# Optimization experiments

Measured on AMD Instinct MI355X. Metric: run time of the kernel, lower is better.

## Reference

```python
import jax, jax.numpy as jnp
import numpy as np

Q, C, T, D_IN, D_H = 512, 512, 128, 512, 256


def setup_inputs() -> dict:
    key = jax.random.key(0)
    ks = jax.random.split(key, 8)
    s_in = 1.0 / np.sqrt(D_IN)
    s_h = 1.0 / np.sqrt(D_H)
    return {
        "audio": jax.random.normal(ks[0], (Q, T, D_IN), jnp.float32),
        "video": jax.random.normal(ks[1], (C, T, D_IN), jnp.float32),
        "a_w1": jax.random.normal(ks[2], (D_IN, D_H), jnp.float32) * s_in,
        "a_b1": jnp.zeros((D_H,), jnp.float32),
        "a_w2": jax.random.normal(ks[3], (D_H, D_H), jnp.float32) * s_h,
        "a_b2": jnp.zeros((D_H,), jnp.float32),
        "v_w1": jax.random.normal(ks[4], (D_IN, D_H), jnp.float32) * s_in,
        "v_b1": jnp.zeros((D_H,), jnp.float32),
        "v_w2": jax.random.normal(ks[5], (D_H, D_H), jnp.float32) * s_h,
        "v_b2": jnp.zeros((D_H,), jnp.float32),
        "W": jax.random.normal(ks[6], (D_H, D_H), jnp.float32) * s_h,
        "max_lag": 4,
    }


def _mlp(x, w1, b1, w2, b2):
    # Linear -> ReLU -> Linear
    h = jnp.maximum(x @ w1 + b1, 0.0)
    return h @ w2 + b2


def reference(audio, video, a_w1, a_b1, a_w2, a_b2,
              v_w1, v_b1, v_w2, v_b2, W, max_lag):
    a = _mlp(audio, a_w1, a_b1, a_w2, a_b2)   # [Q, T, D_H]
    v = _mlp(video, v_w1, v_b1, v_w2, v_b2)   # [C, T, D_H]
    # roll along time commutes with the per-frame linear map, so project once
    pv = jnp.einsum('ctd,df->ctf', v, W)      # [C, T, D_H]
    best = None
    for delta in range(-max_lag, max_lag + 1):
        shifted = jnp.roll(pv, delta, axis=1)
        score = jnp.einsum('qtd,ctd->qc', a, shifted)  # [Q, C]
        best = score if best is None else jnp.maximum(best, score)
    return best
```

## Files before the change

### kernel.cpp

```cpp
#include <hip/hip_runtime.h>
#include <cstdint>
#include <cstddef>

typedef __attribute__((ext_vector_type(8))) short frag8;
typedef __attribute__((ext_vector_type(4))) float f32x4;

static __device__ __forceinline__ unsigned short f2bf(float f) {
    unsigned int u = __float_as_uint(f);
    u += 0x7fffu + ((u >> 16) & 1u);
    return (unsigned short)(u >> 16);
}

static __device__ __forceinline__ void gll16(const void* g, void* l) {
    __builtin_amdgcn_global_load_lds(
        (const __attribute__((address_space(1))) unsigned int*)g,
        (__attribute__((address_space(3))) unsigned int*)l, 16, 0, 0);
}

#define CST 136

template<int AMODE, bool RELU>
__global__ __launch_bounds__(256, 2)
void gemm_mlp(const void* __restrict__ A0, const void* __restrict__ A1,
              const unsigned short* __restrict__ B0, const unsigned short* __restrict__ B1,
              const float* __restrict__ bias0, const float* __restrict__ bias1,
              unsigned short* __restrict__ C0, unsigned short* __restrict__ C1,
              int ldA, int kLen)
{
    __shared__ __align__(16) char smem[CST * 128 * 2];
    unsigned short* As = (unsigned short*)smem;
    unsigned short* Bs = (unsigned short*)(smem + (AMODE == 0 ? 10240 : 8192));
    unsigned short* Cst = (unsigned short*)smem;

    const void* Av = blockIdx.z ? A1 : A0;
    const unsigned short* Bt = blockIdx.z ? B1 : B0;
    const float* bias = blockIdx.z ? bias1 : bias0;
    unsigned short* Cv = blockIdx.z ? C1 : C0;

    const int t    = threadIdx.x;
    const int wave = t >> 6;
    const int lane = t & 63;
    const int quad = lane >> 4;
    const int l15  = lane & 15;
    const int wm   = (wave >> 1) * 64;
    const int wn   = (wave & 1) * 64;
    const int m0   = blockIdx.y * 128;
    const int n0   = blockIdx.x * 128;

    const int rowL = (wave << 5) + (lane >> 2);
    const int qL   = (lane & 3) ^ ((lane >> 3) & 3);
    const size_t offB0 = (size_t)(n0 + rowL) * kLen + qL * 8;
    const size_t offA0 = (size_t)(m0 + rowL) * ldA + qL * 8;
    const int swz = quad ^ ((l15 >> 1) & 3);

    f32x4 acc[4][4];
    #pragma unroll
    for (int i = 0; i < 4; ++i)
        #pragma unroll
        for (int j = 0; j < 4; ++j)
            acc[i][j] = (f32x4){0.f, 0.f, 0.f, 0.f};

    for (int k0 = 0; k0 < kLen; k0 += 32) {
        gll16(Bt + offB0 + k0, &Bs[wave * 1024]);
        gll16(Bt + offB0 + (size_t)16 * kLen + k0, &Bs[wave * 1024 + 512]);
        if (AMODE == 1) {
            const unsigned short* A = (const unsigned short*)Av;
            gll16(A + offA0 + k0, &As[wave * 1024]);
            gll16(A + offA0 + (size_t)16 * ldA + k0, &As[wave * 1024 + 512]);
        } else {
            const float* A = (const float*)Av;
            #pragma unroll
            for (int p = 0; p < 4; ++p) {
                int idx = p * 256 + t;
                int row = idx >> 3;
                int col = (idx & 7) * 4;
                const float4 v = *(const float4*)(A + (size_t)(m0 + row) * ldA + (k0 + col));
                unsigned int u0 = (unsigned int)f2bf(v.x) | ((unsigned int)f2bf(v.y) << 16);
                unsigned int u1 = (unsigned int)f2bf(v.z) | ((unsigned int)f2bf(v.w) << 16);
                uint2 pk; pk.x = u0; pk.y = u1;
                *(uint2*)&As[row * 40 + col] = pk;
            }
        }
        __syncthreads();

        frag8 af[4], bf[4];
        #pragma unroll
        for (int i = 0; i < 4; ++i) {
            const int row = wm + i * 16 + l15;
            if (AMODE == 0)
                af[i] = *(const frag8*)&As[row * 40 + quad * 8];
            else
                af[i] = *(const frag8*)&As[(row * 4 + swz) * 8];
        }
        #pragma unroll
        for (int j = 0; j < 4; ++j) {
            const int row = wn + j * 16 + l15;
            bf[j] = *(const frag8*)&Bs[(row * 4 + swz) * 8];
        }
        #pragma unroll
        for (int i = 0; i < 4; ++i)
            #pragma unroll
            for (int j = 0; j < 4; ++j)
                acc[i][j] = __builtin_amdgcn_mfma_f32_16x16x32_bf16(af[i], bf[j], acc[i][j], 0, 0, 0);
        __syncthreads();
    }

    #pragma unroll
    for (int i = 0; i < 4; ++i) {
        const int rl = wm + i * 16 + quad * 4;
        #pragma unroll
        for (int j = 0; j < 4; ++j) {
            const int cl = wn + j * 16 + l15;
            const float bv = bias[n0 + cl];
            #pragma unroll
            for (int r = 0; r < 4; ++r) {
                float val = acc[i][j][r] + bv;
                if (RELU) val = fmaxf(val, 0.0f);
                Cst[(rl + r) * CST + cl] = f2bf(val);
            }
        }
    }
    __syncthreads();
    #pragma unroll
    for (int u = 0; u < 8; ++u) {
        const int c   = u * 256 + t;
        const int row = c >> 4;
        const int c8  = (c & 15) * 8;
        uint4 v = *(const uint4*)&Cst[row * CST + c8];
        *(uint4*)&Cv[(size_t)(m0 + row) * 256 + n0 + c8] = v;
    }
}

__global__ __launch_bounds__(256, 2)
void gemm_corr(const unsigned short* __restrict__ A, const unsigned short* __restrict__ B,
               float* __restrict__ partial)
{
    __shared__ __align__(16) unsigned short As[128 * 64];
    __shared__ __align__(16) unsigned short Bs[128 * 64];

    const int t    = threadIdx.x;
    const int wave = t >> 6;
    const int lane = t & 63;
    const int quad = lane >> 4;
    const int l15  = lane & 15;
    const int wm   = (wave >> 1) * 64;
    const int wn   = (wave & 1) * 64;
    const int m0   = blockIdx.y * 128;
    const int n0   = blockIdx.x * 128;

    const int z      = blockIdx.z;
    const int kStart = (z & 3) * 8192;
    const int delta  = (z >> 2) - 4;
    const int koff   = (32768 - 256 * delta) & 32767;

    const int rowL = (wave << 5) + (lane >> 3);
    const int qL   = (lane & 7) ^ ((lane >> 3) & 7);
    const size_t aBase = (size_t)(m0 + rowL) * 32768 + qL * 8;
    const size_t bBase = (size_t)(n0 + rowL) * 32768 + qL * 8;
    unsigned short* AsW = As + wave * 2048;
    unsigned short* BsW = Bs + wave * 2048;
    const int swz = l15 & 7;

    f32x4 acc[4][4];
    #pragma unroll
    for (int i = 0; i < 4; ++i)
        #pragma unroll
        for (int j = 0; j < 4; ++j)
            acc[i][j] = (f32x4){0.f, 0.f, 0.f, 0.f};

    for (int k0 = 0; k0 < 8192; k0 += 64) {
        const int kA = kStart + k0;
        const int kB = (kA + koff) & 32767;
        #pragma unroll
        for (int p = 0; p < 4; ++p) {
            gll16(A + aBase + (size_t)(p * 8) * 32768 + kA, AsW + p * 512);
            gll16(B + bBase + (size_t)(p * 8) * 32768 + kB, BsW + p * 512);
        }
        __syncthreads();

        frag8 af[2][4], bf[2][4];
        #pragma unroll
        for (int i = 0; i < 4; ++i) {
            const int row = wm + i * 16 + l15;
            #pragma unroll
            for (int kh = 0; kh < 2; ++kh)
                af[kh][i] = *(const frag8*)&As[row * 64 + (((kh * 4 + quad) ^ swz) * 8)];
        }
        #pragma unroll
        for (int j = 0; j < 4; ++j) {
            const int row = wn + j * 16 + l15;
            #pragma unroll
            for (int kh = 0; kh < 2; ++kh)
                bf[kh][j] = *(const frag8*)&Bs[row * 64 + (((kh * 4 + quad) ^ swz) * 8)];
        }
        #pragma unroll
        for (int kh = 0; kh < 2; ++kh)
            #pragma unroll
            for (int i = 0; i < 4; ++i)
                #pragma unroll
                for (int j = 0; j < 4; ++j)
                    acc[i][j] = __builtin_amdgcn_mfma_f32_16x16x32_bf16(af[kh][i], bf[kh][j], acc[i][j], 0, 0, 0);
        __syncthreads();
    }

    float* C = partial + (size_t)z * 262144;
    #pragma unroll
    for (int i = 0; i < 4; ++i) {
        const int rg = m0 + wm + i * 16 + quad * 4;
        #pragma unroll
        for (int j = 0; j < 4; ++j) {
            const int cg = n0 + wn + j * 16 + l15;
            #pragma unroll
            for (int r = 0; r < 4; ++r)
                C[(size_t)(rg + r) * 512 + cg] = acc[i][j][r];
        }
    }
}

__global__ void prep(const float* __restrict__ a_w1, const float* __restrict__ v_w1,
                     const float* __restrict__ a_w2, const float* __restrict__ v_w2,
                     const float* __restrict__ W, const float* __restrict__ v_b2,
                     unsigned short* __restrict__ aw1T, unsigned short* __restrict__ vw1T,
                     unsigned short* __restrict__ aw2T,
                     unsigned short* __restrict__ WcT, float* __restrict__ bc)
{
    const int b = blockIdx.x;
    __shared__ float tl[32][33];
    __shared__ float wcol[256];
    if (b < 320) {
        const float* src; unsigned short* dst; int R, C, tile;
        if (b < 128)      { src = a_w1; dst = aw1T; R = 512; C = 256; tile = b; }
        else if (b < 256) { src = v_w1; dst = vw1T; R = 512; C = 256; tile = b - 128; }
        else              { src = a_w2; dst = aw2T; R = 256; C = 256; tile = b - 256; }
        const int tilesX = C / 32;
        const int bx = (tile % tilesX) * 32, by = (tile / tilesX) * 32;
        const int tx = threadIdx.x & 31, ty = threadIdx.x >> 5;
        #pragma unroll
        for (int r = ty; r < 32; r += 8)
            tl[r][tx] = src[(size_t)(by + r) * C + bx + tx];
        __syncthreads();
        #pragma unroll
        for (int c = ty; c < 32; c += 8)
            dst[(size_t)(bx + c) * R + by + tx] = f2bf(tl[tx][c]);
    } else {
        const int n = b - 320, k = threadIdx.x;
        wcol[k] = W[(size_t)k * 256 + n];
        __syncthreads();
        float s = 0.f;
        #pragma unroll 8
        for (int d = 0; d < 256; ++d) s += v_w2[(size_t)k * 256 + d] * wcol[d];
        WcT[(size_t)n * 256 + k] = f2bf(s);
        if (k == 0) {
            float tt = 0.f;
            for (int d = 0; d < 256; ++d) tt += v_b2[d] * wcol[d];
            bc[n] = tt;
        }
    }
}

__global__ void reduce_max9(const float* __restrict__ partial, float* __restrict__ out) {
    const int idx = blockIdx.x * blockDim.x + threadIdx.x;
    float best = -3.4e38f;
    #pragma unroll
    for (int dz = 0; dz < 9; ++dz) {
        float s = 0.f;
        #pragma unroll
        for (int ks = 0; ks < 4; ++ks)
            s += partial[((size_t)(dz * 4 + ks) << 18) + idx];
        best = fmaxf(best, s);
    }
    out[idx] = best;
}

extern "C" void kernel_launch(void* const* d_in, const int* in_sizes, int n_in,
                              void* d_out, int out_size, void* d_ws, size_t ws_size,
                              hipStream_t stream) {
    const float* audio = (const float*)d_in[0];
    const float* video = (const float*)d_in[1];
    const float* a_w1  = (const float*)d_in[2];
    const float* a_b1  = (const float*)d_in[3];
    const float* a_w2  = (const float*)d_in[4];
    const float* a_b2  = (const float*)d_in[5];
    const float* v_w1  = (const float*)d_in[6];
    const float* v_b1  = (const float*)d_in[7];
    const float* v_w2  = (const float*)d_in[8];
    const float* v_b2  = (const float*)d_in[9];
    const float* Wm    = (const float*)d_in[10];

    char* ws = (char*)d_ws;
    unsigned short* aw1T = (unsigned short*)(ws + 0);
    unsigned short* vw1T = (unsigned short*)(ws + 262144);
    unsigned short* aw2T = (unsigned short*)(ws + 524288);
    unsigned short* WcT  = (unsigned short*)(ws + 655360);
    float*          bc   = (float*)(ws + 786432);
    unsigned short* a_bf = (unsigned short*)(ws + 1048576);
    unsigned short* pv   = (unsigned short*)(ws + 34603008);
    unsigned short* h_a  = (unsigned short*)(ws + 68157440);
    unsigned short* h_v  = (unsigned short*)(ws + 101711872);
    float* partial       = (float*)(ws + 68157440);
    float* out = (float*)d_out;

    prep<<<dim3(576), 256, 0, stream>>>(a_w1, v_w1, a_w2, v_w2, Wm, v_b2,
                                        aw1T, vw1T, aw2T, WcT, bc);
    gemm_mlp<0, true><<<dim3(2, 512, 2), 256, 0, stream>>>(
        audio, video, aw1T, vw1T, a_b1, v_b1, h_a, h_v, 512, 512);
    gemm_mlp<1, false><<<dim3(2, 512, 2), 256, 0, stream>>>(
        h_a, h_v, aw2T, WcT, a_b2, bc, a_bf, pv, 256, 256);
    gemm_corr<<<dim3(4, 4, 36), 256, 0, stream>>>(a_bf, pv, partial);
    reduce_max9<<<dim3(1024), 256, 0, stream>>>(partial, out);
}
```

Before: 543.5 us.

## Fuse both MLP layers into one kernel keeping hidden tile in LDS

Replaces the two separate GEMM launches for the MLP layers with one kernel. Each block computes a 64-row tile across the full 256-wide hidden dimension, keeps the ReLU output in shared memory, and feeds it straight into the second GEMM. This removes the global write and re-read of the hidden activations and one launch. It also uses a 64-wide K step and a cheaper round-half-up bf16 conversion built with perm instructions. In exchange, each block uses more LDS (about 75 KB), which may lower occupancy, and the A-tile reuse per block changes.

Result: faster. 499.7 us (-8.1%).

```diff
diff --git a/kernel.cpp b/kernel.cpp
--- a/kernel.cpp
+++ b/kernel.cpp
@@ -5,10 +5,8 @@
 typedef __attribute__((ext_vector_type(8))) short frag8;
 typedef __attribute__((ext_vector_type(4))) float f32x4;
 
-static __device__ __forceinline__ unsigned short f2bf(float f) {
-    unsigned int u = __float_as_uint(f);
-    u += 0x7fffu + ((u >> 16) & 1u);
-    return (unsigned short)(u >> 16);
+static __device__ __forceinline__ unsigned short f2bf_r(float f) {
+    return (unsigned short)((__float_as_uint(f) + 0x8000u) >> 16);
 }
 
 static __device__ __forceinline__ void gll16(const void* g, void* l) {
@@ -17,41 +15,38 @@
         (__attribute__((address_space(3))) unsigned int*)l, 16, 0, 0);
 }
 
-#define CST 136
-
-template<int AMODE, bool RELU>
 __global__ __launch_bounds__(256, 2)
-void gemm_mlp(const void* __restrict__ A0, const void* __restrict__ A1,
-              const unsigned short* __restrict__ B0, const unsigned short* __restrict__ B1,
-              const float* __restrict__ bias0, const float* __restrict__ bias1,
-              unsigned short* __restrict__ C0, unsigned short* __restrict__ C1,
-              int ldA, int kLen)
+void mlp_fused(const float* __restrict__ X0, const float* __restrict__ X1,
+               const unsigned short* __restrict__ W1T0, const unsigned short* __restrict__ W1T1,
+               const float* __restrict__ b1v0, const float* __restrict__ b1v1,
+               const unsigned short* __restrict__ W2T0, const unsigned short* __restrict__ W2T1,
+               const float* __restrict__ b2v0, const float* __restrict__ b2v1,
+               unsigned short* __restrict__ O0, unsigned short* __restrict__ O1)
 {
-    __shared__ __align__(16) char smem[CST * 128 * 2];
-    unsigned short* As = (unsigned short*)smem;
-    unsigned short* Bs = (unsigned short*)(smem + (AMODE == 0 ? 10240 : 8192));
-    unsigned short* Cst = (unsigned short*)smem;
-
-    const void* Av = blockIdx.z ? A1 : A0;
-    const unsigned short* Bt = blockIdx.z ? B1 : B0;
-    const float* bias = blockIdx.z ? bias1 : bias0;
-    unsigned short* Cv = blockIdx.z ? C1 : C0;
+    __shared__ __align__(16) unsigned short As[64 * 72];
+    __shared__ __align__(16) unsigned short Bs[256 * 64];
+    __shared__ __align__(16) unsigned short hs[64 * 264];
+
+    const int mod = blockIdx.y;
+    const float* X = mod ? X1 : X0;
+    const unsigned short* W1T = mod ? W1T1 : W1T0;
+    const unsigned short* W2T = mod ? W2T1 : W2T0;
+    const float* b1 = mod ? b1v1 : b1v0;
+    const float* b2 = mod ? b2v1 : b2v0;
+    unsigned short* O = mod ? O1 : O0;
 
     const int t    = threadIdx.x;
     const int wave = t >> 6;
     const int lane = t & 63;
     const int quad = lane >> 4;
     const int l15  = lane & 15;
-    const int wm   = (wave >> 1) * 64;
-    const int wn   = (wave & 1) * 64;
-    const int m0   = blockIdx.y * 128;
-    const int n0   = blockIdx.x * 128;
-
-    const int rowL = (wave << 5) + (lane >> 2);
-    const int qL   = (lane & 3) ^ ((lane >> 3) & 3);
-    const size_t offB0 = (size_t)(n0 + rowL) * kLen + qL * 8;
-    const size_t offA0 = (size_t)(m0 + rowL) * ldA + qL * 8;
-    const int swz = quad ^ ((l15 >> 1) & 3);
+    const int m0   = blockIdx.x * 64;
+
+    const int rowB = lane >> 3;
+    const int qB   = (lane & 7) ^ rowB;
+    const int nRowBase = wave * 64 + rowB;
+    unsigned short* BsW = Bs + wave * 4096;
+    const int swz = l15 & 7;
 
     f32x4 acc[4][4];
     #pragma unroll
@@ -60,74 +55,119 @@
         for (int j = 0; j < 4; ++j)
             acc[i][j] = (f32x4){0.f, 0.f, 0.f, 0.f};
 
-    for (int k0 = 0; k0 < kLen; k0 += 32) {
-        gll16(Bt + offB0 + k0, &Bs[wave * 1024]);
-        gll16(Bt + offB0 + (size_t)16 * kLen + k0, &Bs[wave * 1024 + 512]);
-        if (AMODE == 1) {
-            const unsigned short* A = (const unsigned short*)Av;
-            gll16(A + offA0 + k0, &As[wave * 1024]);
-            gll16(A + offA0 + (size_t)16 * ldA + k0, &As[wave * 1024 + 512]);
-        } else {
-            const float* A = (const float*)Av;
-            #pragma unroll
-            for (int p = 0; p < 4; ++p) {
-                int idx = p * 256 + t;
-                int row = idx >> 3;
-                int col = (idx & 7) * 4;
-                const float4 v = *(const float4*)(A + (size_t)(m0 + row) * ldA + (k0 + col));
-                unsigned int u0 = (unsigned int)f2bf(v.x) | ((unsigned int)f2bf(v.y) << 16);
-                unsigned int u1 = (unsigned int)f2bf(v.z) | ((unsigned int)f2bf(v.w) << 16);
-                uint2 pk; pk.x = u0; pk.y = u1;
-                *(uint2*)&As[row * 40 + col] = pk;
-            }
-        }
-        __syncthreads();
-
-        frag8 af[4], bf[4];
+    for (int k0 = 0; k0 < 512; k0 += 64) {
+        #pragma unroll
+        for (int p = 0; p < 4; ++p) {
+            const int idx = p * 256 + t;
+            const int row = idx >> 4;
+            const int col = (idx & 15) * 4;
+            const float4 v = *(const float4*)(X + (size_t)(m0 + row) * 512 + k0 + col);
+            const unsigned int a0 = __float_as_uint(v.x) + 0x8000u;
+            const unsigned int a1 = __float_as_uint(v.y) + 0x8000u;
+            const unsigned int a2 = __float_as_uint(v.z) + 0x8000u;
+            const unsigned int a3 = __float_as_uint(v.w) + 0x8000u;
+            uint2 pk;
+            pk.x = __builtin_amdgcn_perm(a1, a0, 0x07060302u);
+            pk.y = __builtin_amdgcn_perm(a3, a2, 0x07060302u);
+            *(uint2*)&As[row * 72 + col] = pk;
+        }
+        #pragma unroll
+        for (int p = 0; p < 8; ++p)
+            gll16(W1T + (size_t)(nRowBase + p * 8) * 512 + qB * 8 + k0, BsW + p * 512);
+        __syncthreads();
+
+        frag8 af[2][4], bf[2][4];
+        #pragma unroll
+        for (int i = 0; i < 4; ++i)
+            #pragma unroll
+            for (int kh = 0; kh < 2; ++kh)
+                af[kh][i] = *(const frag8*)&As[(i * 16 + l15) * 72 + kh * 32 + quad * 8];
+        #pragma unroll
+        for (int j = 0; j < 4; ++j) {
+            const int row = wave * 64 + j * 16 + l15;
+            #pragma unroll
+            for (int kh = 0; kh < 2; ++kh)
+                bf[kh][j] = *(const frag8*)&Bs[row * 64 + (((kh * 4 + quad) ^ swz) * 8)];
+        }
+        #pragma unroll
+        for (int kh = 0; kh < 2; ++kh)
+            #pragma unroll
+            for (int i = 0; i < 4; ++i)
+                #pragma unroll
+                for (int j = 0; j < 4; ++j)
+                    acc[i][j] = __builtin_amdgcn_mfma_f32_16x16x32_bf16(af[kh][i], bf[kh][j], acc[i][j], 0, 0, 0);
+        __syncthreads();
+    }
+
+    #pragma unroll
+    for (int j = 0; j < 4; ++j) {
+        const int col = wave * 64 + j * 16 + l15;
+        const float bv = b1[col];
         #pragma unroll
         for (int i = 0; i < 4; ++i) {
-            const int row = wm + i * 16 + l15;
-            if (AMODE == 0)
-                af[i] = *(const frag8*)&As[row * 40 + quad * 8];
-            else
-                af[i] = *(const frag8*)&As[(row * 4 + swz) * 8];
-        }
+            const int rl = i * 16 + quad * 4;
+            #pragma unroll
+            for (int r = 0; r < 4; ++r)
+                hs[(rl + r) * 264 + col] = f2bf_r(fmaxf(acc[i][j][r] + bv, 0.0f));
+        }
+    }
+    __syncthreads();
+
+    #pragma unroll
+    for (int i = 0; i < 4; ++i)
+        #pragma unroll
+        for (int j = 0; j < 4; ++j)
+            acc[i][j] = (f32x4){0.f, 0.f, 0.f, 0.f};
+
+    for (int k0 = 0; k0 < 256; k0 += 64) {
+        #pragma unroll
+        for (int p = 0; p < 8; ++p)
+            gll16(W2T + (size_t)(nRowBase + p * 8) * 256 + qB * 8 + k0, BsW + p * 512);
+        __syncthreads();
+
+        frag8 af[2][4], bf[2][4];
+        #pragma unroll
+        for (int i = 0; i < 4; ++i)
+            #pragma unroll
+            for (int kh = 0; kh < 2; ++kh)
+                af[kh][i] = *(const frag8*)&hs[(i * 16 + l15) * 264 + k0 + kh * 32 + quad * 8];
         #pragma unroll
         for (int j = 0; j < 4; ++j) {
-            const int row = wn + j * 16 + l15;
-            bf[j] = *(const frag8*)&Bs[(row * 4 + swz) * 8];
-        }
-        #pragma unroll
-        for (int i = 0; i < 4; ++i)
-            #pragma unroll
-            for (int j = 0; j < 4; ++j)
-                acc[i][j] = __builtin_amdgcn_mfma_f32_16x16x32_bf16(af[i], bf[j], acc[i][j], 0, 0, 0);
-        __syncthreads();
-    }
-
-    #pragma unroll
-    for (int i = 0; i < 4; ++i) {
-        const int rl = wm + i * 16 + quad * 4;
-        #pragma unroll
-        for (int j = 0; j < 4; ++j) {
-            const int cl = wn + j * 16 + l15;
-            const float bv = bias[n0 + cl];
-            #pragma unroll
-            for (int r = 0; r < 4; ++r) {
-                float val = acc[i][j][r] + bv;
-                if (RELU) val = fmaxf(val, 0.0f);
-                Cst[(rl + r) * CST + cl] = f2bf(val);
-            }
+            const int row = wave * 64 + j * 16 + l15;
+            #pragma unroll
+            for (int kh = 0; kh < 2; ++kh)
+                bf[kh][j] = *(const frag8*)&Bs[row * 64 + (((kh * 4 + quad) ^ swz) * 8)];
+        }
+        #pragma unroll
+        for (int kh = 0; kh < 2; ++kh)
+            #pragma unroll
+            for (int i = 0; i < 4; ++i)
+                #pragma unroll
+                for (int j = 0; j < 4; ++j)
+                    acc[i][j] = __builtin_amdgcn_mfma_f32_16x16x32_bf16(af[kh][i], bf[kh][j], acc[i][j], 0, 0, 0);
+        __syncthreads();
+    }
+
+    #pragma unroll
+    for (int j = 0; j < 4; ++j) {
+        const int col = wave * 64 + j * 16 + l15;
+        const float bv = b2[col];
+        #pragma unroll
+        for (int i = 0; i < 4; ++i) {
+            const int rl = i * 16 + quad * 4;
+            #pragma unroll
+            for (int r = 0; r < 4; ++r)
+                hs[(rl + r) * 264 + col] = f2bf_r(acc[i][j][r] + bv);
         }
     }
     __syncthreads();
     #pragma unroll
     for (int u = 0; u < 8; ++u) {
-        const int c   = u * 256 + t;
-        const int row = c >> 4;
-        const int c8  = (c & 15) * 8;
-        uint4 v = *(const uint4*)&Cst[row * CST + c8];
-        *(uint4*)&Cv[(size_t)(m0 + row) * 256 + n0 + c8] = v;
+        const int chunk = u * 256 + t;
+        const int row = chunk >> 5;
+        const int c16 = (chunk & 31) * 8;
+        uint4 v = *(const uint4*)&hs[row * 264 + c16];
+        *(uint4*)&O[(size_t)(m0 + row) * 256 + c16] = v;
     }
 }
 
@@ -241,7 +281,7 @@
         __syncthreads();
         #pragma unroll
         for (int c = ty; c < 32; c += 8)
-            dst[(size_t)(bx + c) * R + by + tx] = f2bf(tl[tx][c]);
+            dst[(size_t)(bx + c) * R + by + tx] = f2bf_r(tl[tx][c]);
     } else {
         const int n = b - 320, k = threadIdx.x;
         wcol[k] = W[(size_t)k * 256 + n];
@@ -249,7 +289,7 @@
         float s = 0.f;
         #pragma unroll 8
         for (int d = 0; d < 256; ++d) s += v_w2[(size_t)k * 256 + d] * wcol[d];
-        WcT[(size_t)n * 256 + k] = f2bf(s);
+        WcT[(size_t)n * 256 + k] = f2bf_r(s);
         if (k == 0) {
             float tt = 0.f;
             for (int d = 0; d < 256; ++d) tt += v_b2[d] * wcol[d];
@@ -295,17 +335,13 @@
     float*          bc   = (float*)(ws + 786432);
     unsigned short* a_bf = (unsigned short*)(ws + 1048576);
     unsigned short* pv   = (unsigned short*)(ws + 34603008);
-    unsigned short* h_a  = (unsigned short*)(ws + 68157440);
-    unsigned short* h_v  = (unsigned short*)(ws + 101711872);
     float* partial       = (float*)(ws + 68157440);
     float* out = (float*)d_out;
 
     prep<<<dim3(576), 256, 0, stream>>>(a_w1, v_w1, a_w2, v_w2, Wm, v_b2,
                                         aw1T, vw1T, aw2T, WcT, bc);
-    gemm_mlp<0, true><<<dim3(2, 512, 2), 256, 0, stream>>>(
-        audio, video, aw1T, vw1T, a_b1, v_b1, h_a, h_v, 512, 512);
-    gemm_mlp<1, false><<<dim3(2, 512, 2), 256, 0, stream>>>(
-        h_a, h_v, aw2T, WcT, a_b2, bc, a_bf, pv, 256, 256);
+    mlp_fused<<<dim3(1024, 2), 256, 0, stream>>>(
+        audio, video, aw1T, vw1T, a_b1, v_b1, aw2T, WcT, a_b2, bc, a_bf, pv);
     gemm_corr<<<dim3(4, 4, 36), 256, 0, stream>>>(a_bf, pv, partial);
     reduce_max9<<<dim3(1024), 256, 0, stream>>>(partial, out);
 }
```
